# Optimization experiments

Measured on AMD Instinct MI355X. Metric: run time of the kernel, lower is better.

Reference implementation:

```python
import jax, jax.numpy as jnp
import numpy as np

N_DRUG = 50000
N_GENE = 50000
E = 600000
D_IN = 128
D_HID = 64
D_EMB = 32


def setup_inputs() -> dict:
    key = jax.random.key(0)
    ks = jax.random.split(key, 32)
    inp = {}
    inp['x_drug'] = jax.random.normal(ks[0], (N_DRUG, D_IN), jnp.float32)
    inp['x_gene'] = jax.random.normal(ks[1], (N_GENE, D_IN), jnp.float32)
    # per-etype edge lists (src,dst)
    inp['dd_src'] = jax.random.randint(ks[2], (E,), 0, N_DRUG)
    inp['dd_dst'] = jax.random.randint(ks[3], (E,), 0, N_DRUG)
    inp['dg_src'] = jax.random.randint(ks[4], (E,), 0, N_DRUG)
    inp['dg_dst'] = jax.random.randint(ks[5], (E,), 0, N_GENE)
    inp['gd_src'] = jax.random.randint(ks[6], (E,), 0, N_GENE)
    inp['gd_dst'] = jax.random.randint(ks[7], (E,), 0, N_DRUG)
    inp['gg_src'] = jax.random.randint(ks[8], (E,), 0, N_GENE)
    inp['gg_dst'] = jax.random.randint(ks[9], (E,), 0, N_GENE)
    # layer-1 per-relation weights (in -> hidden) and per-ntype biases
    s1 = 1.0 / np.sqrt(D_IN)
    inp['W1_dd'] = jax.random.normal(ks[10], (D_IN, D_HID), jnp.float32) * s1
    inp['W1_dg'] = jax.random.normal(ks[11], (D_IN, D_HID), jnp.float32) * s1
    inp['W1_gd'] = jax.random.normal(ks[12], (D_IN, D_HID), jnp.float32) * s1
    inp['W1_gg'] = jax.random.normal(ks[13], (D_IN, D_HID), jnp.float32) * s1
    inp['b1_drug'] = jnp.zeros((D_HID,), jnp.float32)
    inp['b1_gene'] = jnp.zeros((D_HID,), jnp.float32)
    # layer-2 per-relation weights (hidden -> embed) and per-ntype biases
    s2 = 1.0 / np.sqrt(D_HID)
    inp['W2_dd'] = jax.random.normal(ks[14], (D_HID, D_EMB), jnp.float32) * s2
    inp['W2_dg'] = jax.random.normal(ks[15], (D_HID, D_EMB), jnp.float32) * s2
    inp['W2_gd'] = jax.random.normal(ks[16], (D_HID, D_EMB), jnp.float32) * s2
    inp['W2_gg'] = jax.random.normal(ks[17], (D_HID, D_EMB), jnp.float32) * s2
    inp['b2_drug'] = jnp.zeros((D_EMB,), jnp.float32)
    inp['b2_gene'] = jnp.zeros((D_EMB,), jnp.float32)
    return inp


def _rel_mean(x_src, W, src, dst, n_dst):
    # transform-then-gather (efficient when out_dim <= in_dim), segment-mean over dst
    m = (x_src @ W)[src]                                  # [E, out]
    s = jax.ops.segment_sum(m, dst, num_segments=n_dst)   # [n_dst, out]
    deg = jax.ops.segment_sum(jnp.ones((src.shape[0],), m.dtype), dst, num_segments=n_dst)
    return s / jnp.maximum(deg, 1.0)[:, None]


def _rgcn_layer(xd, xg, Wdd, Wdg, Wgd, Wgg, bd, bg,
                dd_src, dd_dst, dg_src, dg_dst, gd_src, gd_dst, gg_src, gg_dst, act):
    hd = (_rel_mean(xd, Wdd, dd_src, dd_dst, N_DRUG)
          + _rel_mean(xg, Wgd, gd_src, gd_dst, N_DRUG) + bd)
    hg = (_rel_mean(xd, Wdg, dg_src, dg_dst, N_GENE)
          + _rel_mean(xg, Wgg, gg_src, gg_dst, N_GENE) + bg)
    if act:
        hd = jax.nn.relu(hd)
        hg = jax.nn.relu(hg)
    return hd, hg


def reference(x_drug, x_gene, dd_src, dd_dst, dg_src, dg_dst, gd_src, gd_dst,
              gg_src, gg_dst, W1_dd, W1_dg, W1_gd, W1_gg, b1_drug, b1_gene,
              W2_dd, W2_dg, W2_gd, W2_gg, b2_drug, b2_gene):
    hd, hg = _rgcn_layer(x_drug, x_gene, W1_dd, W1_dg, W1_gd, W1_gg, b1_drug, b1_gene,
                         dd_src, dd_dst, dg_src, dg_dst, gd_src, gd_dst, gg_src, gg_dst, True)
    hd, hg = _rgcn_layer(hd, hg, W2_dd, W2_dg, W2_gd, W2_gg, b2_drug, b2_gene,
                         dd_src, dd_dst, dg_src, dg_dst, gd_src, gd_dst, gg_src, gg_dst, False)
    # concatenate per-ntype embeddings: rows [0:N_DRUG]=drug, [N_DRUG:]=gene
    return jnp.concatenate([hd, hg], axis=0)
```

## Files before the change

### kernel.cpp

```cpp
#include <hip/hip_runtime.h>
#include <hip/hip_bf16.h>

#define N_NODE 50000
#define NEDGE  600000
#define NRANGE 128
#define RSZ    391
#define CAPB   6144
#define CHUNK  4096
#define NBLK1  147

typedef __hip_bfloat16 bf16;
typedef __attribute__((ext_vector_type(8))) short short8;
typedef __attribute__((ext_vector_type(4))) float floatx4;

__device__ __forceinline__ short f2s(float f) {
    bf16 t = __float2bfloat16(f);
    return *(short*)&t;
}
__device__ __forceinline__ unsigned pk2(float lo, float hi) {
    return ((unsigned)(unsigned short)f2s(lo)) | (((unsigned)(unsigned short)f2s(hi)) << 16);
}
__device__ __forceinline__ void acc2(float& a, float& b, unsigned w, float m) {
    a += m * __uint_as_float(w << 16);
    b += m * __uint_as_float(w & 0xFFFF0000u);
}


__global__ __launch_bounds__(256) void k_part(
    const int* __restrict__ d0, const int* __restrict__ s0,
    const int* __restrict__ d1, const int* __restrict__ s1,
    const int* __restrict__ d2, const int* __restrict__ s2,
    const int* __restrict__ d3, const int* __restrict__ s3,
    int* __restrict__ gcur, unsigned* __restrict__ gpart)
{
    __shared__ int hcur[NRANGE];
    __shared__ int delta[NRANGE];
    __shared__ int sc[256];
    __shared__ unsigned buf[CHUNK];
    int bid = blockIdx.x;
    int rel = bid / NBLK1;
    int c   = bid - rel * NBLK1;
    int tid = threadIdx.x;
    const int* dp = rel == 0 ? d0 : rel == 1 ? d1 : rel == 2 ? d2 : d3;
    const int* sp = rel == 0 ? s0 : rel == 1 ? s1 : rel == 2 ? s2 : s3;
    int e0 = c * CHUNK;
    int e1 = min(e0 + CHUNK, NEDGE);
    int cnt_chunk = e1 - e0;

    if (tid < NRANGE) hcur[tid] = 0;
    __syncthreads();
    for (int e = e0 + tid; e < e1; e += 256)
        atomicAdd(&hcur[dp[e] / RSZ], 1);
    __syncthreads();
    int v = (tid < NRANGE) ? hcur[tid] : 0;
    sc[tid] = v;
    __syncthreads();
    for (int d = 1; d < NRANGE; d <<= 1) {
        int t = (tid >= d && tid < NRANGE) ? sc[tid - d] : 0;
        __syncthreads();
        sc[tid] += t;
        __syncthreads();
    }
    if (tid < NRANGE) {
        int start = sc[tid] - v;
        int bg    = rel * NRANGE + tid;
        int resv  = atomicAdd(&gcur[bg], v);
        delta[tid] = bg * CAPB + resv - start;
        hcur[tid]  = start;
    }
    __syncthreads();
    for (int e = e0 + tid; e < e1; e += 256) {
        int d = dp[e];
        int b = d / RSZ;
        int p = atomicAdd(&hcur[b], 1);
        buf[p] = ((unsigned)b << 25) | ((unsigned)(d - b * RSZ) << 16) | (unsigned)sp[e];
    }
    __syncthreads();
    for (int i = tid; i < cnt_chunk; i += 256) {
        unsigned key = buf[i];
        gpart[delta[key >> 25] + i] = key;
    }
}

__global__ __launch_bounds__(512) void k_base(
    const int* __restrict__ gcur, int* __restrict__ base_rel)
{
    __shared__ int sc[512];
    int t = threadIdx.x;
    int v = gcur[t];
    sc[t] = v;
    __syncthreads();
    int loc = t & (NRANGE - 1);
    for (int d = 1; d < NRANGE; d <<= 1) {
        int x = (loc >= d) ? sc[t - d] : 0;
        __syncthreads();
        sc[t] += x;
        __syncthreads();
    }
    base_rel[t] = sc[t] - v;
}

__global__ __launch_bounds__(256) void k_csr(
    const unsigned* __restrict__ gpart, const int* __restrict__ gcnt,
    const int* __restrict__ base_rel, int* __restrict__ off, int* __restrict__ edges)
{
    __shared__ int cur[RSZ];
    __shared__ unsigned short stg[CAPB];
    __shared__ int sc[256];
    int bid = blockIdx.x;
    int rel = bid >> 7, r = bid & (NRANGE - 1);
    int tid = threadIdx.x;
    int range0 = r * RSZ;
    int RS = min(RSZ, N_NODE - range0);
    if (RS < 0) RS = 0;
    int count = gcnt[bid];
    int base  = base_rel[bid];
    size_t slot0 = (size_t)bid * CAPB;

    for (int i = tid; i < RSZ; i += 256) cur[i] = 0;
    __syncthreads();
    for (int i = tid; i < count; i += 256)
        atomicAdd(&cur[(gpart[slot0 + i] >> 16) & 0x1FF], 1);
    __syncthreads();
    int vloc[2]; int run = 0;
#pragma unroll
    for (int j = 0; j < 2; j++) {
        int idx = tid * 2 + j;
        int x = (idx < RSZ) ? cur[idx] : 0;
        vloc[j] = x; run += x;
    }
    sc[tid] = run;
    __syncthreads();
    for (int d = 1; d < 256; d <<= 1) {
        int t = (tid >= d) ? sc[tid - d] : 0;
        __syncthreads();
        sc[tid] += t;
        __syncthreads();
    }
    int excl = sc[tid] - run;
    run = excl;
#pragma unroll
    for (int j = 0; j < 2; j++) {
        int idx = tid * 2 + j;
        if (idx < RSZ) { int x = vloc[j]; cur[idx] = run; run += x; }
    }
    __syncthreads();
    for (int i = tid; i < RS; i += 256)
        off[rel * (N_NODE + 1) + range0 + i] = base + cur[i];
    if (r == NRANGE - 1 && tid == 0) off[rel * (N_NODE + 1) + N_NODE] = NEDGE;
    __syncthreads();
    for (int i = tid; i < count; i += 256) {
        unsigned key = gpart[slot0 + i];
        int p = atomicAdd(&cur[(key >> 16) & 0x1FF], 1);
        stg[p] = (unsigned short)(key & 0xFFFFu);
    }
    __syncthreads();
    for (int i = tid; i < count; i += 256)
        edges[rel * NEDGE + base + i] = (int)stg[i];
}

template <int K, int NOUT, bool AFP32>
__global__ __launch_bounds__(256) void k_gemm_pair(
    const void* __restrict__ X0, const void* __restrict__ X1,
    const float* __restrict__ Wa0, const float* __restrict__ Wb0,
    const float* __restrict__ Wa1, const float* __restrict__ Wb1,
    bf16* __restrict__ out0, bf16* __restrict__ out1, int M)
{
    constexpr int NB  = NOUT / 16;
    constexpr int KC  = K / 32;
    constexpr int NH  = NOUT / 2;
    constexpr int NBL = (NB == 8) ? 3 : 2;
    __shared__ short Wl[KC * NB * 512];

    int sel = blockIdx.y;
    const void*  X  = sel ? X1 : X0;
    const float* Wa = sel ? Wa1 : Wa0;
    const float* Wb = sel ? Wb1 : Wb0;
    bf16*        out = sel ? out1 : out0;

    int tid = threadIdx.x;
    for (int i = tid; i < KC * NB * 512; i += 256) {
        int j  = i & 7;
        int n  = (i >> 3) & 15;
        int q  = (i >> 7) & 3;
        int nb = (i >> 9) & (NB - 1);
        int kc = i >> (9 + NBL);
        int k  = kc * 32 + q * 8 + j;
        int c  = nb * 16 + n;
        float w = (c < NH) ? Wa[k * NH + c] : Wb[k * NH + (c - NH)];
        Wl[i] = f2s(w);
    }
    __syncthreads();

    int lane = tid & 63, wv = tid >> 6;
    int q = lane >> 4, lidx = lane & 15;
    int row0 = blockIdx.x * 64 + wv * 16;
    int rowA = min(row0 + lidx, M - 1);

    floatx4 acc[NB];
#pragma unroll
    for (int nb = 0; nb < NB; nb++) acc[nb] = (floatx4){0.f, 0.f, 0.f, 0.f};

#pragma unroll
    for (int kc = 0; kc < KC; kc++) {
        short8 a;
        if constexpr (AFP32) {
            const float* Xf = (const float*)X + (size_t)rowA * K + kc * 32 + q * 8;
            float4 f0 = *(const float4*)Xf;
            float4 f1 = *(const float4*)(Xf + 4);
            a[0] = f2s(f0.x); a[1] = f2s(f0.y); a[2] = f2s(f0.z); a[3] = f2s(f0.w);
            a[4] = f2s(f1.x); a[5] = f2s(f1.y); a[6] = f2s(f1.z); a[7] = f2s(f1.w);
        } else {
            a = *(const short8*)((const short*)X + (size_t)rowA * K + kc * 32 + q * 8);
        }
#pragma unroll
        for (int nb = 0; nb < NB; nb++) {
            short8 b = *(const short8*)&Wl[((kc * NB + nb) * 64 + lane) * 8];
            acc[nb] = __builtin_amdgcn_mfma_f32_16x16x32_bf16(a, b, acc[nb], 0, 0, 0);
        }
    }
#pragma unroll
    for (int nb = 0; nb < NB; nb++) {
#pragma unroll
        for (int r = 0; r < 4; r++) {
            int row = row0 + q * 4 + r;
            if (row < M)
                out[(size_t)row * NOUT + nb * 16 + lidx] = __float2bfloat16(acc[nb][r]);
        }
    }
}

__device__ __forceinline__ void segc64(
    int begA, int nA, const int* __restrict__ eA,
    int begB, int nB, const int* __restrict__ eB,
    float ia, float ib, int boff,
    int lane, int lgrp, const unsigned* __restrict__ base, float s[8])
{
    int nT = nA + nB;
    for (int e = 0; e < nT; e += 64) {
        int nb = min(64, nT - e);
        int nAr = nA - e;
        int i = e + lane;
        int idx = 0;
        if (i < nT)
            idx = (i < nA) ? eA[begA + i] : (eB[begB + i - nA] + boff);
        for (int j = 0; j < nb; j += 32) {
            int r0 = j + lgrp, r1 = r0 + 8, r2 = r0 + 16, r3 = r0 + 24;
            int sa0 = __shfl(idx, r0);
            int sa1 = __shfl(idx, r1);
            int sa2 = __shfl(idx, r2);
            int sa3 = __shfl(idx, r3);
            float m0 = (r0 < nAr) ? ia : ((r0 < nb) ? ib : 0.f);
            float m1 = (r1 < nAr) ? ia : ((r1 < nb) ? ib : 0.f);
            float m2 = (r2 < nAr) ? ia : ((r2 < nb) ? ib : 0.f);
            float m3 = (r3 < nAr) ? ia : ((r3 < nb) ? ib : 0.f);
            uint4 w0 = *(const uint4*)(base + (size_t)sa0 * 64);
            uint4 w1 = *(const uint4*)(base + (size_t)sa1 * 64);
            uint4 w2 = *(const uint4*)(base + (size_t)sa2 * 64);
            uint4 w3 = *(const uint4*)(base + (size_t)sa3 * 64);
            acc2(s[0], s[1], w0.x, m0); acc2(s[2], s[3], w0.y, m0);
            acc2(s[4], s[5], w0.z, m0); acc2(s[6], s[7], w0.w, m0);
            acc2(s[0], s[1], w1.x, m1); acc2(s[2], s[3], w1.y, m1);
            acc2(s[4], s[5], w1.z, m1); acc2(s[6], s[7], w1.w, m1);
            acc2(s[0], s[1], w2.x, m2); acc2(s[2], s[3], w2.y, m2);
            acc2(s[4], s[5], w2.z, m2); acc2(s[6], s[7], w2.w, m2);
            acc2(s[0], s[1], w3.x, m3); acc2(s[2], s[3], w3.y, m3);
            acc2(s[4], s[5], w3.z, m3); acc2(s[6], s[7], w3.w, m3);
        }
    }
}

__global__ __launch_bounds__(256) void k_gather64x2(
    const bf16* __restrict__ m1,
    const int* __restrict__ offA0, const int* __restrict__ eA0,
    const int* __restrict__ offB0, const int* __restrict__ eB0,
    const float* __restrict__ bias0, bf16* __restrict__ out0,
    const int* __restrict__ offA1, const int* __restrict__ eA1,
    const int* __restrict__ offB1, const int* __restrict__ eB1,
    const float* __restrict__ bias1, bf16* __restrict__ out1)
{
    int gw   = (blockIdx.x * 256 + threadIdx.x) >> 6;
    int lane = threadIdx.x & 63;
    int half = (gw >= N_NODE);
    int wid  = gw - (half ? N_NODE : 0);
    const int* offA = half ? offA1 : offA0;
    const int* eA   = half ? eA1   : eA0;
    const int* offB = half ? offB1 : offB0;
    const int* eB   = half ? eB1   : eB0;
    const float* bias = half ? bias1 : bias0;
    bf16* out = half ? out1 : out0;
    int col = half ? 64 : 0;

    int lgrp = lane >> 3, lidx = lane & 7;
    const unsigned* base = (const unsigned*)m1 + (col >> 1) + lidx * 4;

    int begA = offA[wid], endA = offA[wid + 1];
    int begB = offB[wid], endB = offB[wid + 1];
    int nA = endA - begA, nB = endB - begB;
    float ia = 1.f / (float)max(nA, 1);
    float ib = 1.f / (float)max(nB, 1);

    float s[8] = {0.f,0.f,0.f,0.f,0.f,0.f,0.f,0.f};
    segc64(begA, nA, eA, begB, nB, eB, ia, ib, N_NODE, lane, lgrp, base, s);
#pragma unroll
    for (int k = 0; k < 8; k++) {
        s[k] += __shfl_xor(s[k], 8);
        s[k] += __shfl_xor(s[k], 16);
        s[k] += __shfl_xor(s[k], 32);
    }
    if (lane < 8) {
        float h[8];
#pragma unroll
        for (int k = 0; k < 8; k++)
            h[k] = fmaxf(s[k] + bias[lidx * 8 + k], 0.f);
        uint4 v;
        v.x = pk2(h[0], h[1]); v.y = pk2(h[2], h[3]);
        v.z = pk2(h[4], h[5]); v.w = pk2(h[6], h[7]);
        *(uint4*)(out + (size_t)wid * 64 + lidx * 8) = v;
    }
}

__device__ __forceinline__ void segc32(
    int begA, int nA, const int* __restrict__ eA,
    int begB, int nB, const int* __restrict__ eB,
    float ia, float ib, int boff,
    int lane, int lgrp, const unsigned* __restrict__ base, float s[4])
{
    int nT = nA + nB;
    for (int e = 0; e < nT; e += 64) {
        int nb = min(64, nT - e);
        int nAr = nA - e;
        int i = e + lane;
        int idx = 0;
        if (i < nT)
            idx = (i < nA) ? eA[begA + i] : (eB[begB + i - nA] + boff);
        for (int j = 0; j < nb; j += 32) {
            int r0 = j + lgrp, r1 = r0 + 8, r2 = r0 + 16, r3 = r0 + 24;
            int sa0 = __shfl(idx, r0);
            int sa1 = __shfl(idx, r1);
            int sa2 = __shfl(idx, r2);
            int sa3 = __shfl(idx, r3);
            float m0 = (r0 < nAr) ? ia : ((r0 < nb) ? ib : 0.f);
            float m1 = (r1 < nAr) ? ia : ((r1 < nb) ? ib : 0.f);
            float m2 = (r2 < nAr) ? ia : ((r2 < nb) ? ib : 0.f);
            float m3 = (r3 < nAr) ? ia : ((r3 < nb) ? ib : 0.f);
            uint2 w0 = *(const uint2*)(base + (size_t)sa0 * 32);
            uint2 w1 = *(const uint2*)(base + (size_t)sa1 * 32);
            uint2 w2 = *(const uint2*)(base + (size_t)sa2 * 32);
            uint2 w3 = *(const uint2*)(base + (size_t)sa3 * 32);
            acc2(s[0], s[1], w0.x, m0); acc2(s[2], s[3], w0.y, m0);
            acc2(s[0], s[1], w1.x, m1); acc2(s[2], s[3], w1.y, m1);
            acc2(s[0], s[1], w2.x, m2); acc2(s[2], s[3], w2.y, m2);
            acc2(s[0], s[1], w3.x, m3); acc2(s[2], s[3], w3.y, m3);
        }
    }
}

__global__ __launch_bounds__(256) void k_gather32x2(
    const bf16* __restrict__ m1,
    const int* __restrict__ offA0, const int* __restrict__ eA0,
    const int* __restrict__ offB0, const int* __restrict__ eB0,
    const float* __restrict__ bias0, float* __restrict__ out0,
    const int* __restrict__ offA1, const int* __restrict__ eA1,
    const int* __restrict__ offB1, const int* __restrict__ eB1,
    const float* __restrict__ bias1, float* __restrict__ out1)
{
    int gw   = (blockIdx.x * 256 + threadIdx.x) >> 6;
    int lane = threadIdx.x & 63;
    int half = (gw >= N_NODE);
    int wid  = gw - (half ? N_NODE : 0);
    const int* offA = half ? offA1 : offA0;
    const int* eA   = half ? eA1   : eA0;
    const int* offB = half ? offB1 : offB0;
    const int* eB   = half ? eB1   : eB0;
    const float* bias = half ? bias1 : bias0;
    float* out = half ? out1 : out0;
    int col = half ? 32 : 0;

    int lgrp = lane >> 3, lidx = lane & 7;
    const unsigned* base = (const unsigned*)m1 + (col >> 1) + lidx * 2;

    int begA = offA[wid], endA = offA[wid + 1];
    int begB = offB[wid], endB = offB[wid + 1];
    int nA = endA - begA, nB = endB - begB;
    float ia = 1.f / (float)max(nA, 1);
    float ib = 1.f / (float)max(nB, 1);

    float s[4] = {0.f, 0.f, 0.f, 0.f};
    segc32(begA, nA, eA, begB, nB, eB, ia, ib, N_NODE, lane, lgrp, base, s);
#pragma unroll
    for (int k = 0; k < 4; k++) {
        s[k] += __shfl_xor(s[k], 8);
        s[k] += __shfl_xor(s[k], 16);
        s[k] += __shfl_xor(s[k], 32);
    }
    if (lane < 8) {
        float4 v;
        v.x = s[0] + bias[lidx * 4 + 0];
        v.y = s[1] + bias[lidx * 4 + 1];
        v.z = s[2] + bias[lidx * 4 + 2];
        v.w = s[3] + bias[lidx * 4 + 3];
        *(float4*)(out + (size_t)wid * 32 + lidx * 4) = v;
    }
}

extern "C" void kernel_launch(void* const* d_in, const int* in_sizes, int n_in,
                              void* d_out, int out_size, void* d_ws, size_t ws_size,
                              hipStream_t stream)
{
    const float* xd = (const float*)d_in[0];
    const float* xg = (const float*)d_in[1];
    const int* dd_src = (const int*)d_in[2];  const int* dd_dst = (const int*)d_in[3];
    const int* dg_src = (const int*)d_in[4];  const int* dg_dst = (const int*)d_in[5];
    const int* gd_src = (const int*)d_in[6];  const int* gd_dst = (const int*)d_in[7];
    const int* gg_src = (const int*)d_in[8];  const int* gg_dst = (const int*)d_in[9];
    const float* W1dd = (const float*)d_in[10];
    const float* W1dg = (const float*)d_in[11];
    const float* W1gd = (const float*)d_in[12];
    const float* W1gg = (const float*)d_in[13];
    const float* b1d  = (const float*)d_in[14];
    const float* b1g  = (const float*)d_in[15];
    const float* W2dd = (const float*)d_in[16];
    const float* W2dg = (const float*)d_in[17];
    const float* W2gd = (const float*)d_in[18];
    const float* W2gg = (const float*)d_in[19];
    const float* b2d  = (const float*)d_in[20];
    const float* b2g  = (const float*)d_in[21];
    float* out = (float*)d_out;

    int* gcur     = (int*)d_ws;
    int* base_rel = gcur + 512;
    int* off      = base_rel + 512;
    int* edges    = off + 4 * (N_NODE + 1);
    bf16* md1     = (bf16*)(edges + 4 * NEDGE);
    bf16* mg1     = md1 + (size_t)N_NODE * 128;
    bf16* hd      = mg1 + (size_t)N_NODE * 128;
    bf16* hg      = hd + (size_t)N_NODE * 64;
    bf16* md2     = md1;
    bf16* mg2     = md1 + (size_t)N_NODE * 64;
    unsigned* gpart = (unsigned*)md1;

    hipMemsetAsync(gcur, 0, 512 * sizeof(int), stream);
    k_part<<<4 * NBLK1, 256, 0, stream>>>(
        dd_dst, dd_src, gd_dst, gd_src, dg_dst, dg_src, gg_dst, gg_src, gcur, gpart);
    k_base<<<1, 512, 0, stream>>>(gcur, base_rel);
    k_csr<<<512, 256, 0, stream>>>(gpart, gcur, base_rel, off, edges);

    const int* off_dd = off + 0 * (N_NODE + 1);
    const int* off_gd = off + 1 * (N_NODE + 1);
    const int* off_dg = off + 2 * (N_NODE + 1);
    const int* off_gg = off + 3 * (N_NODE + 1);
    const int* e_dd = edges + 0 * NEDGE;
    const int* e_gd = edges + 1 * NEDGE;
    const int* e_dg = edges + 2 * NEDGE;
    const int* e_gg = edges + 3 * NEDGE;

    dim3 gemm_grid((N_NODE + 63) / 64, 2);
    int gather_grid = 2 * N_NODE / 4;

    k_gemm_pair<128, 128, true><<<gemm_grid, 256, 0, stream>>>(
        xd, xg, W1dd, W1dg, W1gd, W1gg, md1, mg1, N_NODE);
    k_gather64x2<<<gather_grid, 256, 0, stream>>>(
        md1,
        off_dd, e_dd, off_gd, e_gd, b1d, hd,
        off_dg, e_dg, off_gg, e_gg, b1g, hg);

    k_gemm_pair<64, 64, false><<<gemm_grid, 256, 0, stream>>>(
        hd, hg, W2dd, W2dg, W2gd, W2gg, md2, mg2, N_NODE);
    k_gather32x2<<<gather_grid, 256, 0, stream>>>(
        md2,
        off_dd, e_dd, off_gd, e_gd, b2d, out,
        off_dg, e_dg, off_gg, e_gg, b2g, out + (size_t)N_NODE * 32);
}
```

Baseline: 353.7 us.

## Assign small thread groups per destination node in gather kernels

Replaces the wave-per-node segment gathers with 8-lane (layer 1) and 4-lane (layer 2) groups per destination node. Each lane reads edge indices directly and accumulates a 16-byte slice of the row, which removes the shuffles and cross-lane reductions. This also cuts idle lanes for low-degree nodes, since the average degree is about 12. The cost is more redundant index loads per group and less memory parallelism per node when degree is high.

Result: faster. 338.5 us (-4.3%).

```diff
diff --git a/kernel.cpp b/kernel.cpp
--- a/kernel.cpp
+++ b/kernel.cpp
@@ -230,47 +230,39 @@
     }
 }
 
-__device__ __forceinline__ void segc64(
-    int begA, int nA, const int* __restrict__ eA,
-    int begB, int nB, const int* __restrict__ eB,
-    float ia, float ib, int boff,
-    int lane, int lgrp, const unsigned* __restrict__ base, float s[8])
-{
-    int nT = nA + nB;
-    for (int e = 0; e < nT; e += 64) {
-        int nb = min(64, nT - e);
-        int nAr = nA - e;
-        int i = e + lane;
-        int idx = 0;
-        if (i < nT)
-            idx = (i < nA) ? eA[begA + i] : (eB[begB + i - nA] + boff);
-        for (int j = 0; j < nb; j += 32) {
-            int r0 = j + lgrp, r1 = r0 + 8, r2 = r0 + 16, r3 = r0 + 24;
-            int sa0 = __shfl(idx, r0);
-            int sa1 = __shfl(idx, r1);
-            int sa2 = __shfl(idx, r2);
-            int sa3 = __shfl(idx, r3);
-            float m0 = (r0 < nAr) ? ia : ((r0 < nb) ? ib : 0.f);
-            float m1 = (r1 < nAr) ? ia : ((r1 < nb) ? ib : 0.f);
-            float m2 = (r2 < nAr) ? ia : ((r2 < nb) ? ib : 0.f);
-            float m3 = (r3 < nAr) ? ia : ((r3 < nb) ? ib : 0.f);
-            uint4 w0 = *(const uint4*)(base + (size_t)sa0 * 64);
-            uint4 w1 = *(const uint4*)(base + (size_t)sa1 * 64);
-            uint4 w2 = *(const uint4*)(base + (size_t)sa2 * 64);
-            uint4 w3 = *(const uint4*)(base + (size_t)sa3 * 64);
-            acc2(s[0], s[1], w0.x, m0); acc2(s[2], s[3], w0.y, m0);
-            acc2(s[4], s[5], w0.z, m0); acc2(s[6], s[7], w0.w, m0);
-            acc2(s[0], s[1], w1.x, m1); acc2(s[2], s[3], w1.y, m1);
-            acc2(s[4], s[5], w1.z, m1); acc2(s[6], s[7], w1.w, m1);
-            acc2(s[0], s[1], w2.x, m2); acc2(s[2], s[3], w2.y, m2);
-            acc2(s[4], s[5], w2.z, m2); acc2(s[6], s[7], w2.w, m2);
-            acc2(s[0], s[1], w3.x, m3); acc2(s[2], s[3], w3.y, m3);
-            acc2(s[4], s[5], w3.z, m3); acc2(s[6], s[7], w3.w, m3);
-        }
-    }
-}
-
-__global__ __launch_bounds__(256) void k_gather64x2(
+template<int ROWU>
+__device__ __forceinline__ void seg_run(
+    int n, const int* __restrict__ ep, float sc,
+    const unsigned* __restrict__ base, float* s)
+{
+    int nfull = n & ~3;
+    for (int i = 0; i < nfull; i += 4) {
+        int e0 = ep[i + 0];
+        int e1 = ep[i + 1];
+        int e2 = ep[i + 2];
+        int e3 = ep[i + 3];
+        uint4 w0 = *(const uint4*)(base + e0 * ROWU);
+        uint4 w1 = *(const uint4*)(base + e1 * ROWU);
+        uint4 w2 = *(const uint4*)(base + e2 * ROWU);
+        uint4 w3 = *(const uint4*)(base + e3 * ROWU);
+        acc2(s[0], s[1], w0.x, sc); acc2(s[2], s[3], w0.y, sc);
+        acc2(s[4], s[5], w0.z, sc); acc2(s[6], s[7], w0.w, sc);
+        acc2(s[0], s[1], w1.x, sc); acc2(s[2], s[3], w1.y, sc);
+        acc2(s[4], s[5], w1.z, sc); acc2(s[6], s[7], w1.w, sc);
+        acc2(s[0], s[1], w2.x, sc); acc2(s[2], s[3], w2.y, sc);
+        acc2(s[4], s[5], w2.z, sc); acc2(s[6], s[7], w2.w, sc);
+        acc2(s[0], s[1], w3.x, sc); acc2(s[2], s[3], w3.y, sc);
+        acc2(s[4], s[5], w3.z, sc); acc2(s[6], s[7], w3.w, sc);
+    }
+    for (int i = nfull; i < n; i++) {
+        int e = ep[i];
+        uint4 w = *(const uint4*)(base + e * ROWU);
+        acc2(s[0], s[1], w.x, sc); acc2(s[2], s[3], w.y, sc);
+        acc2(s[4], s[5], w.z, sc); acc2(s[6], s[7], w.w, sc);
+    }
+}
+
+__global__ __launch_bounds__(256) void k_gather64v2(
     const bf16* __restrict__ m1,
     const int* __restrict__ offA0, const int* __restrict__ eA0,
     const int* __restrict__ offB0, const int* __restrict__ eB0,
@@ -279,85 +271,41 @@
     const int* __restrict__ offB1, const int* __restrict__ eB1,
     const float* __restrict__ bias1, bf16* __restrict__ out1)
 {
-    int gw   = (blockIdx.x * 256 + threadIdx.x) >> 6;
-    int lane = threadIdx.x & 63;
-    int half = (gw >= N_NODE);
-    int wid  = gw - (half ? N_NODE : 0);
+    int tid  = threadIdx.x;
+    int gid  = blockIdx.x * 32 + (tid >> 3);
+    int lidx = tid & 7;
+    int half = (gid >= N_NODE);
+    int wid  = gid - (half ? N_NODE : 0);
     const int* offA = half ? offA1 : offA0;
     const int* eA   = half ? eA1   : eA0;
     const int* offB = half ? offB1 : offB0;
     const int* eB   = half ? eB1   : eB0;
     const float* bias = half ? bias1 : bias0;
     bf16* out = half ? out1 : out0;
-    int col = half ? 64 : 0;
-
-    int lgrp = lane >> 3, lidx = lane & 7;
-    const unsigned* base = (const unsigned*)m1 + (col >> 1) + lidx * 4;
-
-    int begA = offA[wid], endA = offA[wid + 1];
-    int begB = offB[wid], endB = offB[wid + 1];
-    int nA = endA - begA, nB = endB - begB;
+
+    const unsigned* base = (const unsigned*)m1 + (half ? 32 : 0) + lidx * 4;
+
+    int begA = offA[wid], nA = offA[wid + 1] - begA;
+    int begB = offB[wid], nB = offB[wid + 1] - begB;
     float ia = 1.f / (float)max(nA, 1);
     float ib = 1.f / (float)max(nB, 1);
 
     float s[8] = {0.f,0.f,0.f,0.f,0.f,0.f,0.f,0.f};
-    segc64(begA, nA, eA, begB, nB, eB, ia, ib, N_NODE, lane, lgrp, base, s);
-#pragma unroll
-    for (int k = 0; k < 8; k++) {
-        s[k] += __shfl_xor(s[k], 8);
-        s[k] += __shfl_xor(s[k], 16);
-        s[k] += __shfl_xor(s[k], 32);
-    }
-    if (lane < 8) {
-        float h[8];
-#pragma unroll
-        for (int k = 0; k < 8; k++)
-            h[k] = fmaxf(s[k] + bias[lidx * 8 + k], 0.f);
-        uint4 v;
-        v.x = pk2(h[0], h[1]); v.y = pk2(h[2], h[3]);
-        v.z = pk2(h[4], h[5]); v.w = pk2(h[6], h[7]);
-        *(uint4*)(out + (size_t)wid * 64 + lidx * 8) = v;
-    }
-}
-
-__device__ __forceinline__ void segc32(
-    int begA, int nA, const int* __restrict__ eA,
-    int begB, int nB, const int* __restrict__ eB,
-    float ia, float ib, int boff,
-    int lane, int lgrp, const unsigned* __restrict__ base, float s[4])
-{
-    int nT = nA + nB;
-    for (int e = 0; e < nT; e += 64) {
-        int nb = min(64, nT - e);
-        int nAr = nA - e;
-        int i = e + lane;
-        int idx = 0;
-        if (i < nT)
-            idx = (i < nA) ? eA[begA + i] : (eB[begB + i - nA] + boff);
-        for (int j = 0; j < nb; j += 32) {
-            int r0 = j + lgrp, r1 = r0 + 8, r2 = r0 + 16, r3 = r0 + 24;
-            int sa0 = __shfl(idx, r0);
-            int sa1 = __shfl(idx, r1);
-            int sa2 = __shfl(idx, r2);
-            int sa3 = __shfl(idx, r3);
-            float m0 = (r0 < nAr) ? ia : ((r0 < nb) ? ib : 0.f);
-            float m1 = (r1 < nAr) ? ia : ((r1 < nb) ? ib : 0.f);
-            float m2 = (r2 < nAr) ? ia : ((r2 < nb) ? ib : 0.f);
-            float m3 = (r3 < nAr) ? ia : ((r3 < nb) ? ib : 0.f);
-            uint2 w0 = *(const uint2*)(base + (size_t)sa0 * 32);
-            uint2 w1 = *(const uint2*)(base + (size_t)sa1 * 32);
-            uint2 w2 = *(const uint2*)(base + (size_t)sa2 * 32);
-            uint2 w3 = *(const uint2*)(base + (size_t)sa3 * 32);
-            acc2(s[0], s[1], w0.x, m0); acc2(s[2], s[3], w0.y, m0);
-            acc2(s[0], s[1], w1.x, m1); acc2(s[2], s[3], w1.y, m1);
-            acc2(s[0], s[1], w2.x, m2); acc2(s[2], s[3], w2.y, m2);
-            acc2(s[0], s[1], w3.x, m3); acc2(s[2], s[3], w3.y, m3);
-        }
-    }
-}
-
-__global__ __launch_bounds__(256) void k_gather32x2(
-    const bf16* __restrict__ m1,
+    seg_run<64>(nA, eA + begA, ia, base, s);
+    seg_run<64>(nB, eB + begB, ib, base + N_NODE * 64, s);
+
+    float h[8];
+#pragma unroll
+    for (int k = 0; k < 8; k++)
+        h[k] = fmaxf(s[k] + bias[lidx * 8 + k], 0.f);
+    uint4 v;
+    v.x = pk2(h[0], h[1]); v.y = pk2(h[2], h[3]);
+    v.z = pk2(h[4], h[5]); v.w = pk2(h[6], h[7]);
+    *(uint4*)(out + (size_t)wid * 64 + lidx * 8) = v;
+}
+
+__global__ __launch_bounds__(256) void k_gather32v2(
+    const bf16* __restrict__ m2,
     const int* __restrict__ offA0, const int* __restrict__ eA0,
     const int* __restrict__ offB0, const int* __restrict__ eB0,
     const float* __restrict__ bias0, float* __restrict__ out0,
@@ -365,43 +313,42 @@
     const int* __restrict__ offB1, const int* __restrict__ eB1,
     const float* __restrict__ bias1, float* __restrict__ out1)
 {
-    int gw   = (blockIdx.x * 256 + threadIdx.x) >> 6;
-    int lane = threadIdx.x & 63;
-    int half = (gw >= N_NODE);
-    int wid  = gw - (half ? N_NODE : 0);
+    int tid  = threadIdx.x;
+    int gid  = blockIdx.x * 64 + (tid >> 2);
+    int lidx = tid & 3;
+    if (gid >= 2 * N_NODE) return;
+    int half = (gid >= N_NODE);
+    int wid  = gid - (half ? N_NODE : 0);
     const int* offA = half ? offA1 : offA0;
     const int* eA   = half ? eA1   : eA0;
     const int* offB = half ? offB1 : offB0;
     const int* eB   = half ? eB1   : eB0;
     const float* bias = half ? bias1 : bias0;
     float* out = half ? out1 : out0;
-    int col = half ? 32 : 0;
-
-    int lgrp = lane >> 3, lidx = lane & 7;
-    const unsigned* base = (const unsigned*)m1 + (col >> 1) + lidx * 2;
-
-    int begA = offA[wid], endA = offA[wid + 1];
-    int begB = offB[wid], endB = offB[wid + 1];
-    int nA = endA - begA, nB = endB - begB;
+
+    const unsigned* base = (const unsigned*)m2 + (half ? 16 : 0) + lidx * 4;
+
+    int begA = offA[wid], nA = offA[wid + 1] - begA;
+    int begB = offB[wid], nB = offB[wid + 1] - begB;
     float ia = 1.f / (float)max(nA, 1);
     float ib = 1.f / (float)max(nB, 1);
 
-    float s[4] = {0.f, 0.f, 0.f, 0.f};
-    segc32(begA, nA, eA, begB, nB, eB, ia, ib, N_NODE, lane, lgrp, base, s);
-#pragma unroll
-    for (int k = 0; k < 4; k++) {
-        s[k] += __shfl_xor(s[k], 8);
-        s[k] += __shfl_xor(s[k], 16);
-        s[k] += __shfl_xor(s[k], 32);
-    }
-    if (lane < 8) {
-        float4 v;
-        v.x = s[0] + bias[lidx * 4 + 0];
-        v.y = s[1] + bias[lidx * 4 + 1];
-        v.z = s[2] + bias[lidx * 4 + 2];
-        v.w = s[3] + bias[lidx * 4 + 3];
-        *(float4*)(out + (size_t)wid * 32 + lidx * 4) = v;
-    }
+    float s[8] = {0.f,0.f,0.f,0.f,0.f,0.f,0.f,0.f};
+    seg_run<32>(nA, eA + begA, ia, base, s);
+    seg_run<32>(nB, eB + begB, ib, base + N_NODE * 32, s);
+
+    float* o = out + (size_t)wid * 32 + lidx * 8;
+    float4 v0, v1;
+    v0.x = s[0] + bias[lidx * 8 + 0];
+    v0.y = s[1] + bias[lidx * 8 + 1];
+    v0.z = s[2] + bias[lidx * 8 + 2];
+    v0.w = s[3] + bias[lidx * 8 + 3];
+    v1.x = s[4] + bias[lidx * 8 + 4];
+    v1.y = s[5] + bias[lidx * 8 + 5];
+    v1.z = s[6] + bias[lidx * 8 + 6];
+    v1.w = s[7] + bias[lidx * 8 + 7];
+    *(float4*)o = v0;
+    *(float4*)(o + 4) = v1;
 }
 
 extern "C" void kernel_launch(void* const* d_in, const int* in_sizes, int n_in,
@@ -456,18 +403,19 @@
     const int* e_gg = edges + 3 * NEDGE;
 
     dim3 gemm_grid((N_NODE + 63) / 64, 2);
-    int gather_grid = 2 * N_NODE / 4;
+    int g64_grid = (2 * N_NODE) / 32;
+    int g32_grid = (2 * N_NODE + 63) / 64;
 
     k_gemm_pair<128, 128, true><<<gemm_grid, 256, 0, stream>>>(
         xd, xg, W1dd, W1dg, W1gd, W1gg, md1, mg1, N_NODE);
-    k_gather64x2<<<gather_grid, 256, 0, stream>>>(
+    k_gather64v2<<<g64_grid, 256, 0, stream>>>(
         md1,
         off_dd, e_dd, off_gd, e_gd, b1d, hd,
         off_dg, e_dg, off_gg, e_gg, b1g, hg);
 
     k_gemm_pair<64, 64, false><<<gemm_grid, 256, 0, stream>>>(
         hd, hg, W2dd, W2dg, W2gd, W2gg, md2, mg2, N_NODE);
-    k_gather32x2<<<gather_grid, 256, 0, stream>>>(
+    k_gather32v2<<<g32_grid, 256, 0, stream>>>(
         md2,
         off_dd, e_dd, off_gd, e_gd, b2d, out,
         off_dg, e_dg, off_gg, e_gg, b2g, out + (size_t)N_NODE * 32);
```
